# Kernel optimization log

Hardware: AMD Instinct MI355X
Metric: run time of the kernel (lower is better)

The kernel has to match this reference:

```python
import jax, jax.numpy as jnp
import numpy as np

N_EMBD = 768
N_HEAD = 8
B, T = 4, 2048

def setup_inputs() -> dict:
    key = jax.random.key(0)
    k1, k2, k3, k4, k5 = jax.random.split(key, 5)
    C = N_EMBD
    s = 1.0 / np.sqrt(C)
    return {
        "x": jax.random.normal(k1, (B, T, C), dtype=jnp.float32),
        "W_attn": jax.random.normal(k2, (C, 3 * C), dtype=jnp.float32) * s,
        "b_attn": jnp.zeros((3 * C,), dtype=jnp.float32),
        "W_proj": jax.random.normal(k3, (C, C), dtype=jnp.float32) * s,
        "b_proj": jnp.zeros((C,), dtype=jnp.float32),
    }

def reference(x, W_attn, b_attn, W_proj, b_proj):
    Bs, Ts, C = x.shape
    H = N_HEAD
    hs = C // H
    qkv = x @ W_attn + b_attn                      # [B,T,3C]
    q, k, v = jnp.split(qkv, 3, axis=-1)
    # reshape to [B,H,T,hs]
    q = q.reshape(Bs, Ts, H, hs).transpose(0, 2, 1, 3)
    k = k.reshape(Bs, Ts, H, hs).transpose(0, 2, 1, 3)
    v = v.reshape(Bs, Ts, H, hs).transpose(0, 2, 1, 3)
    scale = 1.0 / jnp.sqrt(jnp.float32(hs))
    att = jnp.einsum('bhid,bhjd->bhij', q, k) * scale   # [B,H,T,T]
    mask = jnp.tril(jnp.ones((Ts, Ts), dtype=bool))
    att = jnp.where(mask, att, -jnp.inf)
    m = jnp.max(att, axis=-1, keepdims=True)
    e = jnp.where(mask, jnp.exp(att - m), 0.0)
    # original kernel divides by (sum + 1e-9)
    att = e / (jnp.sum(e, axis=-1, keepdims=True) + 1e-9)
    y = jnp.einsum('bhij,bhjd->bhid', att, v)           # [B,H,T,hs]
    y = y.transpose(0, 2, 1, 3).reshape(Bs, Ts, C)
    return y @ W_proj + b_proj
```

## Files before the change

### kernel.cpp

```cpp
#include <hip/hip_runtime.h>

typedef __bf16 bf16;
typedef __attribute__((ext_vector_type(4))) __bf16 bf16x4;
typedef __attribute__((ext_vector_type(8))) __bf16 bf16x8;
typedef __attribute__((ext_vector_type(4))) float f32x4;

#define B_   4
#define T_   2048
#define C_   768
#define H_   8
#define HS_  96
#define M_   (B_ * T_)
#define QKN_ (3 * C_)

#define NEG_BIG (-1e30f)

#define KSTR 104
#define VSTR 72

__device__ __forceinline__ void gload_lds16(const bf16* g, bf16* l) {
    __builtin_amdgcn_global_load_lds(
        (const __attribute__((address_space(1))) uint32_t*)g,
        (__attribute__((address_space(3))) uint32_t*)l,
        16, 0, 0);
}

__device__ __forceinline__ bf16x8 cvt8(f32x4 v0, f32x4 v1) {
    bf16x8 o;
#pragma unroll
    for (int i = 0; i < 4; ++i) { o[i] = (bf16)v0[i]; o[4 + i] = (bf16)v1[i]; }
    return o;
}

__global__ void transpose_kernel(const float* __restrict__ W, bf16* __restrict__ Wt,
                                 int R, int Cn) {
    __shared__ bf16 tile[32][33];
    int tx = threadIdx.x, ty = threadIdx.y;
    int x  = blockIdx.x * 32 + tx;
    int y0 = blockIdx.y * 32;
#pragma unroll
    for (int j = 0; j < 32; j += 8)
        tile[ty + j][tx] = (bf16)W[(size_t)(y0 + ty + j) * Cn + x];
    __syncthreads();
    int y2 = blockIdx.x * 32;
    int x2 = y0 + tx;
#pragma unroll
    for (int j = 0; j < 32; j += 8)
        Wt[(size_t)(y2 + ty + j) * R + x2] = tile[tx][ty + j];
}

__global__ void sentinel_kernel(float* __restrict__ out, int n) {
    int i = blockIdx.x * 256 + threadIdx.x;
    if (i < n) out[i] = 12345.0f;
}

__global__ __launch_bounds__(256) void convert_bf16_kernel(const float* __restrict__ in,
                                                           bf16* __restrict__ out,
                                                           int n8) {
    int i = blockIdx.x * 256 + threadIdx.x;
    if (i >= n8) return;
    const float* p = in + (size_t)i * 8;
    f32x4 a = *(const f32x4*)p;
    f32x4 b = *(const f32x4*)(p + 4);
    *(bf16x8*)&out[(size_t)i * 8] = cvt8(a, b);
}

#define CONV_BLKS (M_ * C_ / 8 / 256)
#define TA_BX (QKN_ / 32)
#define TA_BLKS (TA_BX * (C_ / 32))
#define TP_BX (C_ / 32)
#define TP_BLKS (TP_BX * (C_ / 32))

__device__ __forceinline__ void transpose_body(bf16 (*tile)[33],
                                               const float* __restrict__ W,
                                               bf16* __restrict__ Wt,
                                               int R, int Cn, int bx, int by, int tid) {
    int tx = tid & 31, ty = tid >> 5;
    int x  = bx * 32 + tx;
    int y0 = by * 32;
#pragma unroll
    for (int j = 0; j < 32; j += 8)
        tile[ty + j][tx] = (bf16)W[(size_t)(y0 + ty + j) * Cn + x];
    __syncthreads();
    int y2 = bx * 32;
    int x2 = y0 + tx;
#pragma unroll
    for (int j = 0; j < 32; j += 8)
        Wt[(size_t)(y2 + ty + j) * R + x2] = tile[tx][ty + j];
}

__global__ __launch_bounds__(256) void prep_kernel(const float* __restrict__ x,
                                                   bf16* __restrict__ xb,
                                                   const float* __restrict__ Wa,
                                                   bf16* __restrict__ Wta,
                                                   const float* __restrict__ Wp,
                                                   bf16* __restrict__ Wtp) {
    __shared__ bf16 tile[32][33];
    int bid = blockIdx.x;
    int tid = threadIdx.x;
    if (bid < CONV_BLKS) {
        int i = bid * 256 + tid;
        const float* p = x + (size_t)i * 8;
        f32x4 a = *(const f32x4*)p;
        f32x4 b = *(const f32x4*)(p + 4);
        *(bf16x8*)&xb[(size_t)i * 8] = cvt8(a, b);
    } else if (bid < CONV_BLKS + TA_BLKS) {
        int t = bid - CONV_BLKS;
        transpose_body(tile, Wa, Wta, C_, QKN_, t % TA_BX, t / TA_BX, tid);
    } else {
        int t = bid - CONV_BLKS - TA_BLKS;
        transpose_body(tile, Wp, Wtp, C_, C_, t % TP_BX, t / TP_BX, tid);
    }
}

#define TILE_ELEMS (128 * 64)

__global__ __launch_bounds__(256) void gemm_qkv(const bf16* __restrict__ A,
                                                const bf16* __restrict__ Bt,
                                                const float* __restrict__ bias,
                                                bf16* __restrict__ Cmat,
                                                bf16* __restrict__ Vt,
                                                int M, int N, int K) {
    __shared__ bf16 lda[2 * TILE_ELEMS];
    __shared__ bf16 ldb[2 * TILE_ELEMS];
    int tid  = threadIdx.x;
    int w    = tid >> 6;
    int lane = tid & 63;
    int col  = lane & 15, quad = lane >> 4;
    int wr   = w >> 1, wc = w & 1;
    int m0   = blockIdx.y * 128, n0 = blockIdx.x * 128;

    int srow = lane >> 3;
    int scol = (lane & 7) * 8;
    const bf16* gA[4]; const bf16* gB[4]; bf16* lA[4]; bf16* lB[4];
#pragma unroll
    for (int i = 0; i < 4; ++i) {
        int seg = w * 4 + i;
        int row = seg * 8 + srow;
        gA[i] = &A[(size_t)(m0 + row) * K + scol];
        gB[i] = &Bt[(size_t)(n0 + row) * K + scol];
        lA[i] = &lda[seg * 512];
        lB[i] = &ldb[seg * 512];
    }

    const f32x4 zero = {0.f, 0.f, 0.f, 0.f};
    f32x4 acc[4][4];
#pragma unroll
    for (int mr = 0; mr < 4; ++mr)
#pragma unroll
        for (int nc = 0; nc < 4; ++nc) acc[mr][nc] = zero;

#pragma unroll
    for (int i = 0; i < 4; ++i) {
        gload_lds16(gA[i], lA[i]);
        gload_lds16(gB[i], lB[i]);
    }
    __syncthreads();

    int cur = 0;
    for (int k0 = 0; k0 < K; k0 += 64) {
        int nxt = cur ^ 1;
        if (k0 + 64 < K) {
#pragma unroll
            for (int i = 0; i < 4; ++i) {
                gload_lds16(gA[i] + k0 + 64, lA[i] + nxt * TILE_ELEMS);
                gload_lds16(gB[i] + k0 + 64, lB[i] + nxt * TILE_ELEMS);
            }
        }
        const bf16* la = &lda[cur * TILE_ELEMS];
        const bf16* lb = &ldb[cur * TILE_ELEMS];
#pragma unroll
        for (int ks = 0; ks < 2; ++ks) {
            bf16x8 af[4], bfr[4];
#pragma unroll
            for (int t = 0; t < 4; ++t) {
                af[t]  = *(const bf16x8*)&la[(wr * 64 + t * 16 + col) * 64 + ks * 32 + quad * 8];
                bfr[t] = *(const bf16x8*)&lb[(wc * 64 + t * 16 + col) * 64 + ks * 32 + quad * 8];
            }
#pragma unroll
            for (int mr = 0; mr < 4; ++mr)
#pragma unroll
                for (int nc = 0; nc < 4; ++nc)
                    acc[mr][nc] = __builtin_amdgcn_mfma_f32_16x16x32_bf16(
                        af[mr], bfr[nc], acc[mr][nc], 0, 0, 0);
        }
        __syncthreads();
        cur = nxt;
    }

#pragma unroll
    for (int nc = 0; nc < 4; ++nc) {
        int n = n0 + wc * 64 + nc * 16 + col;
        float bv = bias[n];
#pragma unroll
        for (int mr = 0; mr < 4; ++mr) {
#pragma unroll
            for (int r = 0; r < 4; ++r) {
                int row = m0 + wr * 64 + mr * 16 + quad * 4 + r;
                Cmat[(size_t)row * N + n] = (bf16)(acc[mr][nc][r] + bv);
            }
        }
    }
    if (n0 >= 2 * C_) {
        int batch = m0 >> 11;
        bf16* Vtb = Vt + (size_t)batch * C_ * T_;
        int t0 = (m0 & 2047) + wr * 64;
#pragma unroll
        for (int nc = 0; nc < 4; ++nc) {
            int n  = n0 + wc * 64 + nc * 16 + col;
            int vc = n - 2 * C_;
            float bv = bias[n];
#pragma unroll
            for (int mr = 0; mr < 4; ++mr) {
                int t  = t0 + mr * 16 + quad * 4;
                int tb = t & ~63;
                int a  = (t >> 2) & 15;
                int ts = tb + ((a & 7) << 3) + ((a >> 3) << 2);
                bf16x4 pk = {(bf16)(acc[mr][nc][0] + bv), (bf16)(acc[mr][nc][1] + bv),
                             (bf16)(acc[mr][nc][2] + bv), (bf16)(acc[mr][nc][3] + bv)};
                *(bf16x4*)&Vtb[(size_t)vc * T_ + ts] = pk;
            }
        }
    }
}

__global__ __launch_bounds__(256) void gemm_proj(const bf16* __restrict__ A,
                                                 const bf16* __restrict__ Bt,
                                                 const float* __restrict__ bias,
                                                 float* __restrict__ Cmat,
                                                 int M, int N, int K) {
    __shared__ bf16 lda[2 * TILE_ELEMS];
    __shared__ bf16 ldb[2 * TILE_ELEMS];
    int tid  = threadIdx.x;
    int w    = tid >> 6;
    int lane = tid & 63;
    int col  = lane & 15, quad = lane >> 4;
    int wr   = w >> 1, wc = w & 1;
    int m0   = blockIdx.y * 128, n0 = blockIdx.x * 128;

    int srow = lane >> 3;
    int scol = (lane & 7) * 8;
    const bf16* gA[4]; const bf16* gB[4]; bf16* lA[4]; bf16* lB[4];
#pragma unroll
    for (int i = 0; i < 4; ++i) {
        int seg = w * 4 + i;
        int row = seg * 8 + srow;
        gA[i] = &A[(size_t)(m0 + row) * K + scol];
        gB[i] = &Bt[(size_t)(n0 + row) * K + scol];
        lA[i] = &lda[seg * 512];
        lB[i] = &ldb[seg * 512];
    }

    const f32x4 zero = {0.f, 0.f, 0.f, 0.f};
    f32x4 acc[4][4];
#pragma unroll
    for (int mr = 0; mr < 4; ++mr)
#pragma unroll
        for (int nc = 0; nc < 4; ++nc) acc[mr][nc] = zero;

#pragma unroll
    for (int i = 0; i < 4; ++i) {
        gload_lds16(gA[i], lA[i]);
        gload_lds16(gB[i], lB[i]);
    }
    __syncthreads();

    int cur = 0;
    for (int k0 = 0; k0 < K; k0 += 64) {
        int nxt = cur ^ 1;
        if (k0 + 64 < K) {
#pragma unroll
            for (int i = 0; i < 4; ++i) {
                gload_lds16(gA[i] + k0 + 64, lA[i] + nxt * TILE_ELEMS);
                gload_lds16(gB[i] + k0 + 64, lB[i] + nxt * TILE_ELEMS);
            }
        }
        const bf16* la = &lda[cur * TILE_ELEMS];
        const bf16* lb = &ldb[cur * TILE_ELEMS];
#pragma unroll
        for (int ks = 0; ks < 2; ++ks) {
            bf16x8 af[4], bfr[4];
#pragma unroll
            for (int t = 0; t < 4; ++t) {
                af[t]  = *(const bf16x8*)&la[(wr * 64 + t * 16 + col) * 64 + ks * 32 + quad * 8];
                bfr[t] = *(const bf16x8*)&lb[(wc * 64 + t * 16 + col) * 64 + ks * 32 + quad * 8];
            }
#pragma unroll
            for (int mr = 0; mr < 4; ++mr)
#pragma unroll
                for (int nc = 0; nc < 4; ++nc)
                    acc[mr][nc] = __builtin_amdgcn_mfma_f32_16x16x32_bf16(
                        af[mr], bfr[nc], acc[mr][nc], 0, 0, 0);
        }
        __syncthreads();
        cur = nxt;
    }

#pragma unroll
    for (int nc = 0; nc < 4; ++nc) {
        int n = n0 + wc * 64 + nc * 16 + col;
        float bv = bias[n];
#pragma unroll
        for (int mr = 0; mr < 4; ++mr) {
#pragma unroll
            for (int r = 0; r < 4; ++r) {
                int row = m0 + wr * 64 + mr * 16 + quad * 4 + r;
                Cmat[(size_t)row * N + n] = acc[mr][nc][r] + bv;
            }
        }
    }
}

__global__ __launch_bounds__(256) void attn_kernel(const bf16* __restrict__ qkv,
                                                   const bf16* __restrict__ Vt,
                                                   bf16* __restrict__ y,
                                                   int nGroups) {
    __shared__ bf16 ldsK[64 * KSTR];
    __shared__ bf16 ldsV[96 * VSTR];
    const int bid  = blockIdx.x;
    const int qtt  = 15 - bid / nGroups;
    const int g    = bid % nGroups;
    const int h    = g & 7, b = g >> 3;
    const int tid  = threadIdx.x;
    const int w    = tid >> 6, lane = tid & 63;
    const int col  = lane & 15, quad = lane >> 4;
    const float SCALE2 = 0.10206207261596577f * 1.4426950408889634f;
    const float M0 = 24.0f;
    const f32x4 zero = {0.f, 0.f, 0.f, 0.f};

    const bf16* qkvb = qkv + (size_t)b * T_ * QKN_;
    const bf16* Vtbh = Vt + (size_t)(b * H_ + h) * HS_ * T_;
    bf16* yb  = y + (size_t)b * T_ * C_;

    const int rbaseA = qtt * 128 + w * 16;
    const int rbaseB = rbaseA + 64;

    bf16x8 qfA[3], qfB[3];
#pragma unroll
    for (int c = 0; c < 3; ++c) {
        qfA[c] = *(const bf16x8*)&qkvb[(size_t)(rbaseA + col) * QKN_ + h * HS_ + c * 32 + quad * 8];
        qfB[c] = *(const bf16x8*)&qkvb[(size_t)(rbaseB + col) * QKN_ + h * HS_ + c * 32 + quad * 8];
    }

    const bf16* pK[3]; const bf16* pV[3];
    bf16 *dK[3], *dV[3];
#pragma unroll
    for (int i = 0; i < 3; ++i) {
        int chunk = i * 256 + tid;
        int rK = chunk / 12, cK = chunk - rK * 12;
        pK[i] = qkvb + (size_t)rK * QKN_ + C_ + h * HS_ + cK * 8;
        dK[i] = &ldsK[rK * KSTR + cK * 8];
        int rV = chunk >> 3, cV = chunk & 7;
        pV[i] = Vtbh + (size_t)rV * T_ + cV * 8;
        dV[i] = &ldsV[rV * VSTR + cV * 8];
    }

    f32x4 oA[6], oB[6];
#pragma unroll
    for (int n2 = 0; n2 < 6; ++n2) { oA[n2] = zero; oB[n2] = zero; }
    f32x4 lsumA4 = zero, lsumB4 = zero;

    bf16x8 kreg[3], vreg[3];
#pragma unroll
    for (int i = 0; i < 3; ++i) {
        kreg[i] = *(const bf16x8*)pK[i];
        vreg[i] = *(const bf16x8*)pV[i];
        pK[i] += (size_t)64 * QKN_;
        pV[i] += 64;
    }

    const int njt = 2 * qtt + 2;
    for (int jt = 0; jt < njt; ++jt) {
        const bool aAct = (jt <= 2 * qtt);
        int jb = jt * 64;
        __syncthreads();
#pragma unroll
        for (int i = 0; i < 3; ++i) {
            *(bf16x8*)dK[i] = kreg[i];
            *(bf16x8*)dV[i] = vreg[i];
        }
        __syncthreads();
        if (jt + 1 < njt) {
#pragma unroll
            for (int i = 0; i < 3; ++i) {
                kreg[i] = *(const bf16x8*)pK[i];
                vreg[i] = *(const bf16x8*)pV[i];
                pK[i] += (size_t)64 * QKN_;
                pV[i] += 64;
            }
        }

        f32x4 stA[4], stB[4];
#pragma unroll
        for (int nb = 0; nb < 4; ++nb) {
            stA[nb] = zero; stB[nb] = zero;
#pragma unroll
            for (int c = 0; c < 3; ++c) {
                bf16x8 kf = *(const bf16x8*)&ldsK[(nb * 16 + col) * KSTR + c * 32 + quad * 8];
                if (aAct)
                    stA[nb] = __builtin_amdgcn_mfma_f32_16x16x32_bf16(
                        kf, qfA[c], stA[nb], 0, 0, 0);
                stB[nb] = __builtin_amdgcn_mfma_f32_16x16x32_bf16(
                    kf, qfB[c], stB[nb], 0, 0, 0);
            }
        }

        bf16x8 paloA, pahiA, paloB, pahiB;
        if (aAct) {
            if (jt == 2 * qtt) {
#pragma unroll
                for (int nb = 0; nb < 4; ++nb)
#pragma unroll
                    for (int r = 0; r < 4; ++r) {
                        int jg = jb + nb * 16 + quad * 4 + r;
                        stA[nb][r] = (jg <= rbaseA + col) ? fmaf(stA[nb][r], SCALE2, -M0)
                                                          : NEG_BIG;
                    }
            } else {
#pragma unroll
                for (int nb = 0; nb < 4; ++nb)
#pragma unroll
                    for (int r = 0; r < 4; ++r)
                        stA[nb][r] = fmaf(stA[nb][r], SCALE2, -M0);
            }
#pragma unroll
            for (int nb = 0; nb < 4; ++nb) {
#pragma unroll
                for (int r = 0; r < 4; ++r)
                    stA[nb][r] = exp2f(stA[nb][r]);
                lsumA4 += stA[nb];
            }
#pragma unroll
            for (int r = 0; r < 4; ++r) {
                paloA[r]     = (bf16)stA[0][r];
                paloA[4 + r] = (bf16)stA[2][r];
                pahiA[r]     = (bf16)stA[1][r];
                pahiA[4 + r] = (bf16)stA[3][r];
            }
        }
        if (jt == njt - 1) {
#pragma unroll
            for (int nb = 0; nb < 4; ++nb)
#pragma unroll
                for (int r = 0; r < 4; ++r) {
                    int jg = jb + nb * 16 + quad * 4 + r;
                    stB[nb][r] = (jg <= rbaseB + col) ? fmaf(stB[nb][r], SCALE2, -M0)
                                                      : NEG_BIG;
                }
        } else {
#pragma unroll
            for (int nb = 0; nb < 4; ++nb)
#pragma unroll
                for (int r = 0; r < 4; ++r)
                    stB[nb][r] = fmaf(stB[nb][r], SCALE2, -M0);
        }
#pragma unroll
        for (int nb = 0; nb < 4; ++nb) {
#pragma unroll
            for (int r = 0; r < 4; ++r)
                stB[nb][r] = exp2f(stB[nb][r]);
            lsumB4 += stB[nb];
        }
#pragma unroll
        for (int r = 0; r < 4; ++r) {
            paloB[r]     = (bf16)stB[0][r];
            paloB[4 + r] = (bf16)stB[2][r];
            pahiB[r]     = (bf16)stB[1][r];
            pahiB[4 + r] = (bf16)stB[3][r];
        }

#pragma unroll
        for (int n2 = 0; n2 < 6; ++n2) {
            const bf16* vrow = &ldsV[(n2 * 16 + col) * VSTR];
            bf16x8 vlo = *(const bf16x8*)&vrow[quad * 8];
            bf16x8 vhi = *(const bf16x8*)&vrow[32 + quad * 8];
            if (aAct) {
                oA[n2] = __builtin_amdgcn_mfma_f32_16x16x32_bf16(vlo, paloA, oA[n2], 0, 0, 0);
                oA[n2] = __builtin_amdgcn_mfma_f32_16x16x32_bf16(vhi, pahiA, oA[n2], 0, 0, 0);
            }
            oB[n2] = __builtin_amdgcn_mfma_f32_16x16x32_bf16(vlo, paloB, oB[n2], 0, 0, 0);
            oB[n2] = __builtin_amdgcn_mfma_f32_16x16x32_bf16(vhi, pahiB, oB[n2], 0, 0, 0);
        }
    }

    float lsumA = (lsumA4[0] + lsumA4[1]) + (lsumA4[2] + lsumA4[3]);
    lsumA += __shfl_xor(lsumA, 16, 64);
    lsumA += __shfl_xor(lsumA, 32, 64);
    float linvA = 1.0f / lsumA;
    float lsumB = (lsumB4[0] + lsumB4[1]) + (lsumB4[2] + lsumB4[3]);
    lsumB += __shfl_xor(lsumB, 16, 64);
    lsumB += __shfl_xor(lsumB, 32, 64);
    float linvB = 1.0f / lsumB;
#pragma unroll
    for (int n2 = 0; n2 < 6; ++n2) {
        bf16x4 pkA = {(bf16)(oA[n2][0] * linvA), (bf16)(oA[n2][1] * linvA),
                      (bf16)(oA[n2][2] * linvA), (bf16)(oA[n2][3] * linvA)};
        *(bf16x4*)&yb[(size_t)(rbaseA + col) * C_ + h * HS_ + n2 * 16 + quad * 4] = pkA;
        bf16x4 pkB = {(bf16)(oB[n2][0] * linvB), (bf16)(oB[n2][1] * linvB),
                      (bf16)(oB[n2][2] * linvB), (bf16)(oB[n2][3] * linvB)};
        *(bf16x4*)&yb[(size_t)(rbaseB + col) * C_ + h * HS_ + n2 * 16 + quad * 4] = pkB;
    }
}

extern "C" void kernel_launch(void* const* d_in, const int* in_sizes, int n_in,
                              void* d_out, int out_size, void* d_ws, size_t ws_size,
                              hipStream_t stream) {
    (void)in_sizes; (void)n_in;
    const float* x      = (const float*)d_in[0];
    const float* W_attn = (const float*)d_in[1];
    const float* b_attn = (const float*)d_in[2];
    const float* W_proj = (const float*)d_in[3];
    const float* b_proj = (const float*)d_in[4];
    float* out = (float*)d_out;

    size_t e_wta = (size_t)QKN_ * C_;
    size_t e_wtp = (size_t)C_ * C_;
    size_t a_qkv = e_wta + e_wtp;
    size_t a_vt  = a_qkv + (size_t)M_ * QKN_;
    size_t a_yb  = a_vt + (size_t)M_ * C_;
    size_t needA = (a_yb + (size_t)M_ * C_) * sizeof(bf16);
    size_t b_qkv = e_wta + e_wtp;
    size_t b_vt  = b_qkv + (size_t)T_ * QKN_;
    size_t b_yb  = b_vt + (size_t)T_ * C_;
    size_t needB = (b_yb + (size_t)T_ * C_) * sizeof(bf16);

    if (ws_size >= needA) {
        bf16* Wt_attn = (bf16*)d_ws;
        bf16* Wt_proj = (bf16*)d_ws + e_wta;
        bf16* qkv     = (bf16*)d_ws + a_qkv;
        bf16* Vt      = (bf16*)d_ws + a_vt;
        bf16* yb      = (bf16*)d_ws + a_yb;
        bf16* xb      = yb;
        prep_kernel<<<dim3(CONV_BLKS + TA_BLKS + TP_BLKS), 256, 0, stream>>>(
            x, xb, W_attn, Wt_attn, W_proj, Wt_proj);
        gemm_qkv<<<dim3(QKN_ / 128, M_ / 128), 256, 0, stream>>>(
            xb, Wt_attn, b_attn, qkv, Vt, M_, QKN_, C_);
        attn_kernel<<<dim3(16 * H_ * B_), 256, 0, stream>>>(qkv, Vt, yb, H_ * B_);
        gemm_proj<<<dim3(C_ / 128, M_ / 128), 256, 0, stream>>>(
            yb, Wt_proj, b_proj, out, M_, C_, C_);
    } else if (ws_size >= needB) {
        bf16* Wt_attn = (bf16*)d_ws;
        bf16* Wt_proj = (bf16*)d_ws + e_wta;
        bf16* qkv     = (bf16*)d_ws + b_qkv;
        bf16* Vt      = (bf16*)d_ws + b_vt;
        bf16* yb      = (bf16*)d_ws + b_yb;
        bf16* xb      = yb;
        transpose_kernel<<<dim3(QKN_ / 32, C_ / 32), dim3(32, 8), 0, stream>>>(W_attn, Wt_attn, C_, QKN_);
        transpose_kernel<<<dim3(C_ / 32, C_ / 32), dim3(32, 8), 0, stream>>>(W_proj, Wt_proj, C_, C_);
        for (int b = 0; b < B_; ++b) {
            const float* xf = x + (size_t)b * T_ * C_;
            float* outb     = out + (size_t)b * T_ * C_;
            convert_bf16_kernel<<<dim3(T_ * C_ / 8 / 256), 256, 0, stream>>>(xf, xb, T_ * C_ / 8);
            gemm_qkv<<<dim3(QKN_ / 128, T_ / 128), 256, 0, stream>>>(
                xb, Wt_attn, b_attn, qkv, Vt, T_, QKN_, C_);
            attn_kernel<<<dim3(16 * H_), 256, 0, stream>>>(qkv, Vt, yb, H_);
            gemm_proj<<<dim3(C_ / 128, T_ / 128), 256, 0, stream>>>(
                yb, Wt_proj, b_proj, outb, T_, C_, C_);
        }
    } else {
        sentinel_kernel<<<(out_size + 255) / 256, 256, 0, stream>>>(out, out_size);
    }
}
```

Before: 231.4 us.

## Swizzle GEMM LDS, use waitcnt pipelining, and retile attention to 64-row blocks

In both GEMMs the LDS tiles are XOR-swizzled to avoid bank conflicts, and the per-iteration __syncthreads is replaced by explicit vmcnt waits plus raw barriers so the next tile's prefetch stays in flight. The attention kernel is retiled from 256-thread blocks covering 128 query rows to 128-thread blocks covering 64 rows. This removes the asymmetric causal-skip branch and doubles the grid. It also raises VSTR padding and adds s_setprio around MFMA sections. The risks are correctness of the hand-tuned vmcnt count and reduced K/V reuse per block in attention.

```diff
diff --git a/kernel.cpp b/kernel.cpp
--- a/kernel.cpp
+++ b/kernel.cpp
@@ -16,7 +16,7 @@
 #define NEG_BIG (-1e30f)
 
 #define KSTR 104
-#define VSTR 72
+#define VSTR 88
 
 __device__ __forceinline__ void gload_lds16(const bf16* g, bf16* l) {
     __builtin_amdgcn_global_load_lds(
@@ -131,7 +131,7 @@
     int m0   = blockIdx.y * 128, n0 = blockIdx.x * 128;
 
     int srow = lane >> 3;
-    int scol = (lane & 7) * 8;
+    int scol = ((lane & 7) ^ srow) * 8;
     const bf16* gA[4]; const bf16* gB[4]; bf16* lA[4]; bf16* lB[4];
 #pragma unroll
     for (int i = 0; i < 4; ++i) {
@@ -155,7 +155,6 @@
         gload_lds16(gA[i], lA[i]);
         gload_lds16(gB[i], lB[i]);
     }
-    __syncthreads();
 
     int cur = 0;
     for (int k0 = 0; k0 < K; k0 += 64) {
@@ -166,16 +165,22 @@
                 gload_lds16(gA[i] + k0 + 64, lA[i] + nxt * TILE_ELEMS);
                 gload_lds16(gB[i] + k0 + 64, lB[i] + nxt * TILE_ELEMS);
             }
-        }
+            asm volatile("s_waitcnt vmcnt(8)" ::: "memory");
+        } else {
+            asm volatile("s_waitcnt vmcnt(0)" ::: "memory");
+        }
+        __builtin_amdgcn_s_barrier();
+        __builtin_amdgcn_sched_barrier(0);
         const bf16* la = &lda[cur * TILE_ELEMS];
         const bf16* lb = &ldb[cur * TILE_ELEMS];
 #pragma unroll
         for (int ks = 0; ks < 2; ++ks) {
             bf16x8 af[4], bfr[4];
+            int ca = (((ks * 4 + quad) ^ (col & 7)) * 8);
 #pragma unroll
             for (int t = 0; t < 4; ++t) {
-                af[t]  = *(const bf16x8*)&la[(wr * 64 + t * 16 + col) * 64 + ks * 32 + quad * 8];
-                bfr[t] = *(const bf16x8*)&lb[(wc * 64 + t * 16 + col) * 64 + ks * 32 + quad * 8];
+                af[t]  = *(const bf16x8*)&la[(wr * 64 + t * 16 + col) * 64 + ca];
+                bfr[t] = *(const bf16x8*)&lb[(wc * 64 + t * 16 + col) * 64 + ca];
             }
 #pragma unroll
             for (int mr = 0; mr < 4; ++mr)
@@ -184,7 +189,8 @@
                     acc[mr][nc] = __builtin_amdgcn_mfma_f32_16x16x32_bf16(
                         af[mr], bfr[nc], acc[mr][nc], 0, 0, 0);
         }
-        __syncthreads();
+        __builtin_amdgcn_sched_barrier(0);
+        __builtin_amdgcn_s_barrier();
         cur = nxt;
     }
 
@@ -239,7 +245,7 @@
     int m0   = blockIdx.y * 128, n0 = blockIdx.x * 128;
 
     int srow = lane >> 3;
-    int scol = (lane & 7) * 8;
+    int scol = ((lane & 7) ^ srow) * 8;
     const bf16* gA[4]; const bf16* gB[4]; bf16* lA[4]; bf16* lB[4];
 #pragma unroll
     for (int i = 0; i < 4; ++i) {
@@ -263,7 +269,6 @@
         gload_lds16(gA[i], lA[i]);
         gload_lds16(gB[i], lB[i]);
     }
-    __syncthreads();
 
     int cur = 0;
     for (int k0 = 0; k0 < K; k0 += 64) {
@@ -274,16 +279,22 @@
                 gload_lds16(gA[i] + k0 + 64, lA[i] + nxt * TILE_ELEMS);
                 gload_lds16(gB[i] + k0 + 64, lB[i] + nxt * TILE_ELEMS);
             }
-        }
+            asm volatile("s_waitcnt vmcnt(8)" ::: "memory");
+        } else {
+            asm volatile("s_waitcnt vmcnt(0)" ::: "memory");
+        }
+        __builtin_amdgcn_s_barrier();
+        __builtin_amdgcn_sched_barrier(0);
         const bf16* la = &lda[cur * TILE_ELEMS];
         const bf16* lb = &ldb[cur * TILE_ELEMS];
 #pragma unroll
         for (int ks = 0; ks < 2; ++ks) {
             bf16x8 af[4], bfr[4];
+            int ca = (((ks * 4 + quad) ^ (col & 7)) * 8);
 #pragma unroll
             for (int t = 0; t < 4; ++t) {
-                af[t]  = *(const bf16x8*)&la[(wr * 64 + t * 16 + col) * 64 + ks * 32 + quad * 8];
-                bfr[t] = *(const bf16x8*)&lb[(wc * 64 + t * 16 + col) * 64 + ks * 32 + quad * 8];
+                af[t]  = *(const bf16x8*)&la[(wr * 64 + t * 16 + col) * 64 + ca];
+                bfr[t] = *(const bf16x8*)&lb[(wc * 64 + t * 16 + col) * 64 + ca];
             }
 #pragma unroll
             for (int mr = 0; mr < 4; ++mr)
@@ -292,7 +303,8 @@
                     acc[mr][nc] = __builtin_amdgcn_mfma_f32_16x16x32_bf16(
                         af[mr], bfr[nc], acc[mr][nc], 0, 0, 0);
         }
-        __syncthreads();
+        __builtin_amdgcn_sched_barrier(0);
+        __builtin_amdgcn_s_barrier();
         cur = nxt;
     }
 
@@ -311,14 +323,14 @@
     }
 }
 
-__global__ __launch_bounds__(256) void attn_kernel(const bf16* __restrict__ qkv,
+__global__ __launch_bounds__(128) void attn_kernel(const bf16* __restrict__ qkv,
                                                    const bf16* __restrict__ Vt,
                                                    bf16* __restrict__ y,
                                                    int nGroups) {
     __shared__ bf16 ldsK[64 * KSTR];
     __shared__ bf16 ldsV[96 * VSTR];
     const int bid  = blockIdx.x;
-    const int qtt  = 15 - bid / nGroups;
+    const int qt   = 31 - bid / nGroups;
     const int g    = bid % nGroups;
     const int h    = g & 7, b = g >> 3;
     const int tid  = threadIdx.x;
@@ -332,8 +344,8 @@
     const bf16* Vtbh = Vt + (size_t)(b * H_ + h) * HS_ * T_;
     bf16* yb  = y + (size_t)b * T_ * C_;
 
-    const int rbaseA = qtt * 128 + w * 16;
-    const int rbaseB = rbaseA + 64;
+    const int rbaseA = qt * 64 + w * 16;
+    const int rbaseB = rbaseA + 32;
 
     bf16x8 qfA[3], qfB[3];
 #pragma unroll
@@ -342,17 +354,18 @@
         qfB[c] = *(const bf16x8*)&qkvb[(size_t)(rbaseB + col) * QKN_ + h * HS_ + c * 32 + quad * 8];
     }
 
-    const bf16* pK[3]; const bf16* pV[3];
-    bf16 *dK[3], *dV[3];
-#pragma unroll
-    for (int i = 0; i < 3; ++i) {
-        int chunk = i * 256 + tid;
-        int rK = chunk / 12, cK = chunk - rK * 12;
-        pK[i] = qkvb + (size_t)rK * QKN_ + C_ + h * HS_ + cK * 8;
-        dK[i] = &ldsK[rK * KSTR + cK * 8];
-        int rV = chunk >> 3, cV = chunk & 7;
-        pV[i] = Vtbh + (size_t)rV * T_ + cV * 8;
-        dV[i] = &ldsV[rV * VSTR + cV * 8];
+    const bf16* baseK = qkvb + C_ + h * HS_;
+    const bf16* baseV = Vtbh;
+    int offK[6], dKo[6], offV[6], dVo[6];
+#pragma unroll
+    for (int i = 0; i < 6; ++i) {
+        int ck = i * 128 + tid;
+        int rK = ck / 12, cK = ck - rK * 12;
+        offK[i] = rK * QKN_ + cK * 8;
+        dKo[i]  = rK * KSTR + cK * 8;
+        int rV = ck >> 3, cV = ck & 7;
+        offV[i] = rV * T_ + cV * 8;
+        dVo[i]  = rV * VSTR + cV * 8;
     }
 
     f32x4 oA[6], oB[6];
@@ -360,90 +373,57 @@
     for (int n2 = 0; n2 < 6; ++n2) { oA[n2] = zero; oB[n2] = zero; }
     f32x4 lsumA4 = zero, lsumB4 = zero;
 
-    bf16x8 kreg[3], vreg[3];
-#pragma unroll
-    for (int i = 0; i < 3; ++i) {
-        kreg[i] = *(const bf16x8*)pK[i];
-        vreg[i] = *(const bf16x8*)pV[i];
-        pK[i] += (size_t)64 * QKN_;
-        pV[i] += 64;
-    }
-
-    const int njt = 2 * qtt + 2;
+    bf16x8 kreg[6], vreg[6];
+#pragma unroll
+    for (int i = 0; i < 6; ++i) {
+        kreg[i] = *(const bf16x8*)(baseK + offK[i]);
+        vreg[i] = *(const bf16x8*)(baseV + offV[i]);
+    }
+    baseK += (size_t)64 * QKN_;
+    baseV += 64;
+
+    const int njt = qt + 1;
     for (int jt = 0; jt < njt; ++jt) {
-        const bool aAct = (jt <= 2 * qtt);
         int jb = jt * 64;
         __syncthreads();
 #pragma unroll
-        for (int i = 0; i < 3; ++i) {
-            *(bf16x8*)dK[i] = kreg[i];
-            *(bf16x8*)dV[i] = vreg[i];
+        for (int i = 0; i < 6; ++i) {
+            *(bf16x8*)&ldsK[dKo[i]] = kreg[i];
+            *(bf16x8*)&ldsV[dVo[i]] = vreg[i];
         }
         __syncthreads();
         if (jt + 1 < njt) {
 #pragma unroll
-            for (int i = 0; i < 3; ++i) {
-                kreg[i] = *(const bf16x8*)pK[i];
-                vreg[i] = *(const bf16x8*)pV[i];
-                pK[i] += (size_t)64 * QKN_;
-                pV[i] += 64;
-            }
+            for (int i = 0; i < 6; ++i) {
+                kreg[i] = *(const bf16x8*)(baseK + offK[i]);
+                vreg[i] = *(const bf16x8*)(baseV + offV[i]);
+            }
+            baseK += (size_t)64 * QKN_;
+            baseV += 64;
         }
 
         f32x4 stA[4], stB[4];
+        __builtin_amdgcn_s_setprio(1);
 #pragma unroll
         for (int nb = 0; nb < 4; ++nb) {
             stA[nb] = zero; stB[nb] = zero;
 #pragma unroll
             for (int c = 0; c < 3; ++c) {
                 bf16x8 kf = *(const bf16x8*)&ldsK[(nb * 16 + col) * KSTR + c * 32 + quad * 8];
-                if (aAct)
-                    stA[nb] = __builtin_amdgcn_mfma_f32_16x16x32_bf16(
-                        kf, qfA[c], stA[nb], 0, 0, 0);
-                stB[nb] = __builtin_amdgcn_mfma_f32_16x16x32_bf16(
-                    kf, qfB[c], stB[nb], 0, 0, 0);
-            }
-        }
-
-        bf16x8 paloA, pahiA, paloB, pahiB;
-        if (aAct) {
-            if (jt == 2 * qtt) {
-#pragma unroll
-                for (int nb = 0; nb < 4; ++nb)
-#pragma unroll
-                    for (int r = 0; r < 4; ++r) {
-                        int jg = jb + nb * 16 + quad * 4 + r;
-                        stA[nb][r] = (jg <= rbaseA + col) ? fmaf(stA[nb][r], SCALE2, -M0)
-                                                          : NEG_BIG;
-                    }
-            } else {
-#pragma unroll
-                for (int nb = 0; nb < 4; ++nb)
-#pragma unroll
-                    for (int r = 0; r < 4; ++r)
-                        stA[nb][r] = fmaf(stA[nb][r], SCALE2, -M0);
-            }
-#pragma unroll
-            for (int nb = 0; nb < 4; ++nb) {
-#pragma unroll
-                for (int r = 0; r < 4; ++r)
-                    stA[nb][r] = exp2f(stA[nb][r]);
-                lsumA4 += stA[nb];
-            }
-#pragma unroll
-            for (int r = 0; r < 4; ++r) {
-                paloA[r]     = (bf16)stA[0][r];
-                paloA[4 + r] = (bf16)stA[2][r];
-                pahiA[r]     = (bf16)stA[1][r];
-                pahiA[4 + r] = (bf16)stA[3][r];
-            }
-        }
+                stA[nb] = __builtin_amdgcn_mfma_f32_16x16x32_bf16(kf, qfA[c], stA[nb], 0, 0, 0);
+                stB[nb] = __builtin_amdgcn_mfma_f32_16x16x32_bf16(kf, qfB[c], stB[nb], 0, 0, 0);
+            }
+        }
+        __builtin_amdgcn_s_setprio(0);
+
         if (jt == njt - 1) {
 #pragma unroll
             for (int nb = 0; nb < 4; ++nb)
 #pragma unroll
                 for (int r = 0; r < 4; ++r) {
                     int jg = jb + nb * 16 + quad * 4 + r;
+                    stA[nb][r] = (jg <= rbaseA + col) ? fmaf(stA[nb][r], SCALE2, -M0)
+                                                      : NEG_BIG;
                     stB[nb][r] = (jg <= rbaseB + col) ? fmaf(stB[nb][r], SCALE2, -M0)
                                                       : NEG_BIG;
                 }
@@ -451,36 +431,48 @@
 #pragma unroll
             for (int nb = 0; nb < 4; ++nb)
 #pragma unroll
-                for (int r = 0; r < 4; ++r)
+                for (int r = 0; r < 4; ++r) {
+                    stA[nb][r] = fmaf(stA[nb][r], SCALE2, -M0);
                     stB[nb][r] = fmaf(stB[nb][r], SCALE2, -M0);
-        }
+                }
+        }
+
 #pragma unroll
         for (int nb = 0; nb < 4; ++nb) {
 #pragma unroll
-            for (int r = 0; r < 4; ++r)
+            for (int r = 0; r < 4; ++r) {
+                stA[nb][r] = exp2f(stA[nb][r]);
                 stB[nb][r] = exp2f(stB[nb][r]);
+            }
+            lsumA4 += stA[nb];
             lsumB4 += stB[nb];
         }
+
+        bf16x8 paloA, pahiA, paloB, pahiB;
 #pragma unroll
         for (int r = 0; r < 4; ++r) {
+            paloA[r]     = (bf16)stA[0][r];
+            paloA[4 + r] = (bf16)stA[2][r];
+            pahiA[r]     = (bf16)stA[1][r];
+            pahiA[4 + r] = (bf16)stA[3][r];
             paloB[r]     = (bf16)stB[0][r];
             paloB[4 + r] = (bf16)stB[2][r];
             pahiB[r]     = (bf16)stB[1][r];
             pahiB[4 + r] = (bf16)stB[3][r];
         }
 
+        __builtin_amdgcn_s_setprio(1);
 #pragma unroll
         for (int n2 = 0; n2 < 6; ++n2) {
             const bf16* vrow = &ldsV[(n2 * 16 + col) * VSTR];
             bf16x8 vlo = *(const bf16x8*)&vrow[quad * 8];
             bf16x8 vhi = *(const bf16x8*)&vrow[32 + quad * 8];
-            if (aAct) {
-                oA[n2] = __builtin_amdgcn_mfma_f32_16x16x32_bf16(vlo, paloA, oA[n2], 0, 0, 0);
-                oA[n2] = __builtin_amdgcn_mfma_f32_16x16x32_bf16(vhi, pahiA, oA[n2], 0, 0, 0);
-            }
+            oA[n2] = __builtin_amdgcn_mfma_f32_16x16x32_bf16(vlo, paloA, oA[n2], 0, 0, 0);
+            oA[n2] = __builtin_amdgcn_mfma_f32_16x16x32_bf16(vhi, pahiA, oA[n2], 0, 0, 0);
             oB[n2] = __builtin_amdgcn_mfma_f32_16x16x32_bf16(vlo, paloB, oB[n2], 0, 0, 0);
             oB[n2] = __builtin_amdgcn_mfma_f32_16x16x32_bf16(vhi, pahiB, oB[n2], 0, 0, 0);
         }
+        __builtin_amdgcn_s_setprio(0);
     }
 
     float lsumA = (lsumA4[0] + lsumA4[1]) + (lsumA4[2] + lsumA4[3]);
@@ -535,7 +527,7 @@
             x, xb, W_attn, Wt_attn, W_proj, Wt_proj);
         gemm_qkv<<<dim3(QKN_ / 128, M_ / 128), 256, 0, stream>>>(
             xb, Wt_attn, b_attn, qkv, Vt, M_, QKN_, C_);
-        attn_kernel<<<dim3(16 * H_ * B_), 256, 0, stream>>>(qkv, Vt, yb, H_ * B_);
+        attn_kernel<<<dim3(32 * H_ * B_), 128, 0, stream>>>(qkv, Vt, yb, H_ * B_);
         gemm_proj<<<dim3(C_ / 128, M_ / 128), 256, 0, stream>>>(
             yb, Wt_proj, b_proj, out, M_, C_, C_);
     } else if (ws_size >= needB) {
@@ -553,7 +545,7 @@
             convert_bf16_kernel<<<dim3(T_ * C_ / 8 / 256), 256, 0, stream>>>(xf, xb, T_ * C_ / 8);
             gemm_qkv<<<dim3(QKN_ / 128, T_ / 128), 256, 0, stream>>>(
                 xb, Wt_attn, b_attn, qkv, Vt, T_, QKN_, C_);
-            attn_kernel<<<dim3(16 * H_), 256, 0, stream>>>(qkv, Vt, yb, H_);
+            attn_kernel<<<dim3(32 * H_), 128, 0, stream>>>(qkv, Vt, yb, H_);
             gemm_proj<<<dim3(C_ / 128, T_ / 128), 256, 0, stream>>>(
                 yb, Wt_proj, b_proj, outb, T_, C_, C_);
         }
```

Result: faster. 212.7 us (-8.1%).
